# Kernel tuning notes

Measured on AMD Instinct MI355X. Metric: run time of the kernel, lower is better.

## Reference

```python
import jax, jax.numpy as jnp
import numpy as np

N_NODE = 50000
D = 64
N_HEADS = 8
N_LAYERS = 2
NEG = -1e9
PAD = 0
STDV = 1.0 / np.sqrt(D)


def _l2norm(x, axis):
    n = jnp.sqrt(jnp.sum(x * x, axis=axis, keepdims=True))
    return x / jnp.maximum(n, 1e-12)


def _hgconv(x, theta, bias, edge_index):
    # PyG HypergraphConv (use_attention=False): out = D^-1 H B^-1 H^T (x @ theta) + bias
    xt = x @ theta
    node, hedge = edge_index[0], edge_index[1]
    ones = jnp.ones(node.shape[0], x.dtype)
    Bdeg = jax.ops.segment_sum(ones, hedge, num_segments=N_NODE)   # hyperedge degree
    Ddeg = jax.ops.segment_sum(ones, node, num_segments=N_NODE)    # node degree
    m = jax.ops.segment_sum(xt[node], hedge, num_segments=N_NODE)  # nodes -> hyperedges
    m = m * jnp.where(Bdeg > 0, 1.0 / Bdeg, 0.0)[:, None]
    out = jax.ops.segment_sum(m[hedge], node, num_segments=N_NODE) # hyperedges -> nodes
    out = out * jnp.where(Ddeg > 0, 1.0 / Ddeg, 0.0)[:, None]
    return out + bias


def _mha(x, w, pad_mask, reverse):
    # w: [4, D, D] -> q, k, v, out projections. reverse=True attends to future (triu).
    B, L, d = x.shape
    dk = d // N_HEADS
    split = lambda h: h.reshape(B, L, N_HEADS, dk).transpose(0, 2, 1, 3)
    q, k, v = split(x @ w[0]), split(x @ w[1]), split(x @ w[2])
    scores = jnp.einsum('bhid,bhjd->bhij', q, k) / jnp.sqrt(jnp.asarray(dk, x.dtype))
    tri = jnp.triu(jnp.ones((L, L), bool)) if reverse else jnp.tril(jnp.ones((L, L), bool))
    scores = jnp.where(tri[None, None], scores, NEG)
    scores = jnp.where(pad_mask[:, None, None, :], NEG, scores)
    attn = jax.nn.softmax(scores, axis=-1)
    out = jnp.einsum('bhij,bhjd->bhid', attn, v).transpose(0, 2, 1, 3).reshape(B, L, d)
    return out @ w[3], attn


def _prev_user_mask(seq):
    # scatter -1000 at every user id already seen up to position i (index 0 = PAD column)
    B, L = seq.shape
    tril = jnp.tril(jnp.ones((L, L), bool))
    idx = jnp.where(tril[None], seq[:, None, :], 0)                       # [B,L,L]
    idx = jnp.concatenate([idx, jnp.zeros((B, L, 1), idx.dtype)], axis=2)  # [B,L,L+1]
    b = jnp.arange(B)[:, None, None]
    i = jnp.arange(L)[None, :, None]
    return jnp.zeros((B, L, N_NODE), jnp.float32).at[b, i, idx].set(-1000.0)


def _hg_user(emb_table, gate_w, gate_b, att, att_m, theta, theta_b, edges):
    chans = []
    for c in range(3):
        x = emb_table * jax.nn.sigmoid(emb_table @ gate_w[c] + gate_b[c])  # self-gating
        acc, cur = x, x
        for k in range(N_LAYERS):
            cur = _hgconv(cur, theta[k], theta_b[k], edges[c])
            acc = acc + _l2norm(cur, axis=1)
        chans.append(acc / (N_LAYERS + 1))  # mean over [input, layer1, layer2]
    logits = jnp.stack([jnp.sum(att * (c @ att_m), axis=1) for c in chans], axis=1)  # [N,3]
    score = jax.nn.softmax(logits, axis=-1)
    return sum(score[:, i:i + 1] * chans[i] for i in range(3))


def setup_inputs() -> dict:
    key = jax.random.key(0)
    ks = jax.random.split(key, 20)
    u = lambda k, shp: jax.random.uniform(k, shp, jnp.float32, -STDV, STDV)
    B, L, E = 16, 50, 800000
    return {
        'input_seq': jax.random.randint(ks[0], (B, L), 0, N_NODE),
        'label_seq': jax.random.randint(ks[1], (B, L), 0, N_NODE),
        'input_time': jax.random.randint(ks[2], (B, L), 0, 100000),
        'label_time': jax.random.randint(ks[3], (B, L), 0, 100000),
        'edge_index_g': jax.random.randint(ks[4], (2, E), 0, N_NODE),
        'edge_index_i': jax.random.randint(ks[5], (2, E), 0, N_NODE),
        'edge_index_u': jax.random.randint(ks[6], (2, E), 0, N_NODE),
        'emb_table': u(ks[7], (N_NODE, D)),
        'gate_w': u(ks[8], (3, D, D)),
        'gate_b': u(ks[9], (3, D)),
        'att': u(ks[10], (D,)),
        'att_m': u(ks[11], (D, D)),
        'theta': u(ks[12], (N_LAYERS, D, D)),
        'theta_b': u(ks[13], (N_LAYERS, D)),
        'w_hist': u(ks[14], (4, D, D)),
        'w_fut': u(ks[15], (4, D, D)),
    }


def reference(input_seq, label_seq, input_time, label_time,
              edge_index_g, edge_index_i, edge_index_u,
              emb_table, gate_w, gate_b, att, att_m, theta, theta_b, w_hist, w_fut):
    # input_time / label_time are accepted but unused, as in the original forward.
    HG = _hg_user(emb_table, gate_w, gate_b, att, att_m, theta, theta_b,
                  (edge_index_g, edge_index_i, edge_index_u))
    pad_in = input_seq == PAD
    pad_lb = label_seq == PAD
    past_att_out, past_dist = _mha(HG[input_seq], w_hist, pad_in, reverse=False)
    fut_att_out, fut_dist = _mha(HG[label_seq], w_fut, pad_lb, reverse=True)
    output_past = (past_att_out @ HG.T + _prev_user_mask(input_seq)).reshape(-1, N_NODE)
    future_output = (fut_att_out @ HG.T).reshape(-1, N_NODE)
    return (output_past, future_output, past_dist, fut_dist,
            _l2norm(past_att_out, axis=1), _l2norm(fut_att_out, axis=1))
```

## Files before the change

### kernel.cpp

```cpp
#include <hip/hip_runtime.h>
#include <math.h>

#define N_NODE 50000
#define DD 64
#define NE 800000
#define BB 16
#define LL 50
#define NH 8
#define DK 8
#define NEGV -1e9f
#define NB 49
#define NBLK 256
#define EPB 3125

#define OFF_PDIST 80000000u
#define OFF_FDIST 80320000u
#define OFF_L2P 80640000u
#define OFF_L2F 80691200u

typedef unsigned short ushortt;
typedef __attribute__((ext_vector_type(8))) short bf16x8v;
typedef __attribute__((ext_vector_type(4))) float f32x4v;

__device__ __forceinline__ float b2f(ushortt h) { return __uint_as_float(((unsigned)h) << 16); }
__device__ __forceinline__ ushortt f2b(float f) {
    unsigned u = __float_as_uint(f);
    return (ushortt)((u + 0x7fffu + ((u >> 16) & 1u)) >> 16);
}
__device__ __forceinline__ void acc8(float* a, uint4 x) {
    a[0] += b2f((ushortt)(x.x)); a[1] += b2f((ushortt)(x.x >> 16));
    a[2] += b2f((ushortt)(x.y)); a[3] += b2f((ushortt)(x.y >> 16));
    a[4] += b2f((ushortt)(x.z)); a[5] += b2f((ushortt)(x.z >> 16));
    a[6] += b2f((ushortt)(x.w)); a[7] += b2f((ushortt)(x.w >> 16));
}
__device__ __forceinline__ uint4 pack8(const float* a) {
    uint4 w;
    w.x = (unsigned)f2b(a[0]) | ((unsigned)f2b(a[1]) << 16);
    w.y = (unsigned)f2b(a[2]) | ((unsigned)f2b(a[3]) << 16);
    w.z = (unsigned)f2b(a[4]) | ((unsigned)f2b(a[5]) << 16);
    w.w = (unsigned)f2b(a[6]) | ((unsigned)f2b(a[7]) << 16);
    return w;
}

__global__ void k_zero(float* p, int n) {
    int i = blockIdx.x * 256 + threadIdx.x;
    if (i < n) p[i] = 0.0f;
}

__global__ __launch_bounds__(256) void k_cnt(const int* __restrict__ eg,
                                             const int* __restrict__ ei,
                                             const int* __restrict__ eu,
                                             int* __restrict__ hist) {
    int c = blockIdx.y;
    const int* ed = (c == 0) ? eg : ((c == 1) ? ei : eu);
    int blk = blockIdx.x;
    __shared__ int lc[2 * NB];
    int tid = threadIdx.x;
    for (int j = tid; j < 2 * NB; j += 256) lc[j] = 0;
    __syncthreads();
    int e0 = blk * EPB;
    for (int i = e0 + tid; i < e0 + EPB; i += 256) {
        atomicAdd(&lc[ed[NE + i] >> 10], 1);
        atomicAdd(&lc[NB + (ed[i] >> 10)], 1);
    }
    __syncthreads();
    for (int j = tid; j < 2 * NB; j += 256) {
        int side = (j >= NB);
        int b = side ? (j - NB) : j;
        hist[(((side * 3 + c) * NB) + b) * NBLK + blk] = lc[j];
    }
}

__global__ __launch_bounds__(256) void k_scanH(int* __restrict__ hist, int* __restrict__ bb) {
    int t6 = blockIdx.x;
    int* h = hist + t6 * NB * NBLK;
    __shared__ int part[256];
    int tid = threadIdx.x;
    const int CH = (NB * NBLK) / 256;
    int base = tid * CH;
    int s = 0;
    for (int i = 0; i < CH; i++) s += h[base + i];
    part[tid] = s;
    __syncthreads();
    for (int o = 1; o < 256; o <<= 1) {
        int v = (tid >= o) ? part[tid - o] : 0;
        __syncthreads();
        part[tid] += v;
        __syncthreads();
    }
    int run = (tid == 0) ? 0 : part[tid - 1];
    for (int i = 0; i < CH; i++) {
        int idx = base + i;
        int v = h[idx];
        if ((idx & (NBLK - 1)) == 0) bb[t6 * (NB + 1) + (idx >> 8)] = run;
        h[idx] = run;
        run += v;
    }
    if (tid == 255) bb[t6 * (NB + 1) + NB] = run;
}

__global__ __launch_bounds__(256) void k_part2(const int* __restrict__ eg,
                                               const int* __restrict__ ei,
                                               const int* __restrict__ eu,
                                               const int* __restrict__ hist,
                                               unsigned* __restrict__ poolB,
                                               unsigned* __restrict__ poolD) {
    int c = blockIdx.y;
    const int* ed = (c == 0) ? eg : ((c == 1) ? ei : eu);
    int blk = blockIdx.x;
    __shared__ int curB[NB], curD[NB];
    int tid = threadIdx.x;
    for (int j = tid; j < NB; j += 256) {
        curB[j] = hist[(((0 * 3 + c) * NB) + j) * NBLK + blk];
        curD[j] = hist[(((1 * 3 + c) * NB) + j) * NBLK + blk];
    }
    __syncthreads();
    unsigned* pB = poolB + c * 800000;
    unsigned* pD = poolD + c * 800000;
    int e0 = blk * EPB;
    for (int i = e0 + tid; i < e0 + EPB; i += 256) {
        int n = ed[i], h = ed[NE + i];
        int pb = atomicAdd(&curB[h >> 10], 1);
        pB[pb] = ((unsigned)h << 16) | (unsigned)n;
        int pd = atomicAdd(&curD[n >> 10], 1);
        pD[pd] = ((unsigned)n << 16) | (unsigned)h;
    }
}

__global__ __launch_bounds__(256) void k_bucket(const unsigned* __restrict__ poolB,
                                                const unsigned* __restrict__ poolD,
                                                const int* __restrict__ bb,
                                                int* __restrict__ nbrB3, int* __restrict__ nbrD3,
                                                int* __restrict__ offB3, int* __restrict__ offD3,
                                                float* __restrict__ invB3, float* __restrict__ invD3) {
    int b = blockIdx.x, c = blockIdx.y, side = blockIdx.z;
    const unsigned* pool = (side ? poolD : poolB) + c * 800000;
    int* nbr = (side ? nbrD3 : nbrB3) + c * 800000;
    int* off = (side ? offD3 : offB3) + c * 50001;
    float* inv = (side ? invD3 : invB3) + c * 50000;
    int t6 = side * 3 + c;
    int s0 = bb[t6 * (NB + 1) + b], s1 = bb[t6 * (NB + 1) + b + 1];
    int baseSeg = b << 10;
    __shared__ int cnt[1024];
    __shared__ int ofs[1024];
    __shared__ int part[256];
    int tid = threadIdx.x;
    for (int j = tid; j < 1024; j += 256) cnt[j] = 0;
    __syncthreads();
    for (int i = s0 + tid; i < s1; i += 256)
        atomicAdd(&cnt[(pool[i] >> 16) & 1023], 1);
    __syncthreads();
    int t4 = tid * 4;
    int a0 = cnt[t4], a1 = cnt[t4 + 1], a2 = cnt[t4 + 2], a3 = cnt[t4 + 3];
    part[tid] = a0 + a1 + a2 + a3;
    __syncthreads();
    for (int o = 1; o < 256; o <<= 1) {
        int v = (tid >= o) ? part[tid - o] : 0;
        __syncthreads();
        part[tid] += v;
        __syncthreads();
    }
    int excl = (tid == 0) ? 0 : part[tid - 1];
    ofs[t4] = excl;
    ofs[t4 + 1] = excl + a0;
    ofs[t4 + 2] = excl + a0 + a1;
    ofs[t4 + 3] = excl + a0 + a1 + a2;
    __syncthreads();
    for (int ls = tid; ls < 1024; ls += 256) {
        int seg = baseSeg + ls;
        if (seg < N_NODE) {
            off[seg] = s0 + ofs[ls];
            inv[seg] = cnt[ls] ? 1.0f / (float)cnt[ls] : 0.0f;
        }
    }
    if (b == NB - 1 && tid == 0) off[N_NODE] = NE;
    __syncthreads();
    for (int i = s0 + tid; i < s1; i += 256) {
        unsigned u = pool[i];
        int ls = (u >> 16) & 1023;
        int p = atomicAdd(&ofs[ls], 1);
        nbr[s0 + p] = (int)(u & 0xFFFFu);
    }
}

__global__ __launch_bounds__(256) void k_gate3(const float* __restrict__ emb,
                                               const float* __restrict__ gate_w,
                                               const float* __restrict__ gate_b,
                                               float* __restrict__ cur3,
                                               float* __restrict__ acc3) {
    int c = blockIdx.y;
    const float* W = gate_w + c * 4096;
    const float* bias = gate_b + c * 64;
    float* cur = cur3 + (size_t)c * 3200000;
    float* acc = acc3 + (size_t)c * 3200000;
    __shared__ float sW[64 * 64];
    __shared__ float sx[4][64];
    int tid = threadIdx.x;
    for (int i = tid; i < 4096; i += 256) sW[i] = W[i];
    int r = tid >> 6;
    int d = tid & 63;
    int n = blockIdx.x * 4 + r;
    sx[r][d] = emb[n * DD + d];
    __syncthreads();
    float a = bias[d];
#pragma unroll
    for (int k = 0; k < 64; k++) a += sx[r][k] * sW[k * 64 + d];
    float x = sx[r][d] * (1.0f / (1.0f + expf(-a)));
    cur[n * DD + d] = x;
    acc[n * DD + d] = x;
}

__global__ __launch_bounds__(256) void k_mm64h3(const float* __restrict__ cur3,
                                                const float* __restrict__ W,
                                                ushortt* __restrict__ xt3) {
    int c = blockIdx.y;
    const float* X = cur3 + (size_t)c * 3200000;
    ushortt* Y = xt3 + (size_t)c * 3200000;
    __shared__ float sW[64 * 64];
    __shared__ float sx[4][64];
    int tid = threadIdx.x;
    for (int i = tid; i < 4096; i += 256) sW[i] = W[i];
    int r = tid >> 6;
    int d = tid & 63;
    int n = blockIdx.x * 4 + r;
    sx[r][d] = X[n * DD + d];
    __syncthreads();
    float a = 0.0f;
#pragma unroll
    for (int k = 0; k < 64; k++) a += sx[r][k] * sW[k * 64 + d];
    Y[n * DD + d] = f2b(a);
}

__global__ __launch_bounds__(256) void k_gathB3(const ushortt* __restrict__ xt3,
                                                const int* __restrict__ offB3,
                                                const int* __restrict__ nbrB3,
                                                const float* __restrict__ invB3,
                                                ushortt* __restrict__ m3) {
    int c = blockIdx.y;
    const ushortt* src = xt3 + (size_t)c * 3200000;
    const int* off = offB3 + c * 50001;
    const int* nbr = nbrB3 + c * 800000;
    const float* invSeg = invB3 + c * 50000;
    ushortt* dst = m3 + (size_t)c * 3200000;
    int seg = blockIdx.x * 4 + (threadIdx.x >> 6);
    int lane = threadIdx.x & 63;
    int sub = lane >> 3;
    int c8 = lane & 7;
    int s = off[seg], e = off[seg + 1];
    float a[8] = {0.f, 0.f, 0.f, 0.f, 0.f, 0.f, 0.f, 0.f};
    for (int i = s + sub; i < e; i += 8) {
        uint4 x = ((const uint4*)(src + (size_t)nbr[i] * DD))[c8];
        acc8(a, x);
    }
#pragma unroll
    for (int j = 0; j < 8; j++) {
        a[j] += __shfl_xor(a[j], 8, 64);
        a[j] += __shfl_xor(a[j], 16, 64);
        a[j] += __shfl_xor(a[j], 32, 64);
    }
    if (sub == 0) {
        float sc = invSeg[seg];
        float b[8];
#pragma unroll
        for (int j = 0; j < 8; j++) b[j] = a[j] * sc;
        ((uint4*)(dst + (size_t)seg * DD))[c8] = pack8(b);
    }
}

__global__ __launch_bounds__(256) void k_gathD3(const ushortt* __restrict__ m3,
                                                const int* __restrict__ offD3,
                                                const int* __restrict__ nbrD3,
                                                const float* __restrict__ invD3,
                                                const float* __restrict__ bias,
                                                float* __restrict__ cur3,
                                                float* __restrict__ acc3) {
    int c = blockIdx.y;
    const ushortt* m = m3 + (size_t)c * 3200000;
    const int* off = offD3 + c * 50001;
    const int* nbr = nbrD3 + c * 800000;
    const float* invD = invD3 + c * 50000;
    float* cur = cur3 + (size_t)c * 3200000;
    float* acc = acc3 + (size_t)c * 3200000;
    int seg = blockIdx.x * 4 + (threadIdx.x >> 6);
    int lane = threadIdx.x & 63;
    int sub = lane >> 3;
    int c8 = lane & 7;
    int s = off[seg], e = off[seg + 1];
    float a[8] = {0.f, 0.f, 0.f, 0.f, 0.f, 0.f, 0.f, 0.f};
    for (int i = s + sub; i < e; i += 8) {
        uint4 x = ((const uint4*)(m + (size_t)nbr[i] * DD))[c8];
        acc8(a, x);
    }
#pragma unroll
    for (int j = 0; j < 8; j++) {
        a[j] += __shfl_xor(a[j], 8, 64);
        a[j] += __shfl_xor(a[j], 16, 64);
        a[j] += __shfl_xor(a[j], 32, 64);
    }
    float iD = invD[seg];
    float4 bl = ((const float4*)bias)[c8 * 2];
    float4 bh = ((const float4*)bias)[c8 * 2 + 1];
    float v[8];
    v[0] = a[0] * iD + bl.x; v[1] = a[1] * iD + bl.y;
    v[2] = a[2] * iD + bl.z; v[3] = a[3] * iD + bl.w;
    v[4] = a[4] * iD + bh.x; v[5] = a[5] * iD + bh.y;
    v[6] = a[6] * iD + bh.z; v[7] = a[7] * iD + bh.w;
    float ss = 0.f;
#pragma unroll
    for (int j = 0; j < 8; j++) ss += v[j] * v[j];
    ss += __shfl_xor(ss, 1, 64);
    ss += __shfl_xor(ss, 2, 64);
    ss += __shfl_xor(ss, 4, 64);
    float rn = 1.0f / fmaxf(sqrtf(ss), 1e-12f);
    if (sub == 0) {
        float4 v0 = {v[0], v[1], v[2], v[3]};
        float4 v1 = {v[4], v[5], v[6], v[7]};
        float4* cp = (float4*)(cur + (size_t)seg * DD);
        cp[c8 * 2] = v0;
        cp[c8 * 2 + 1] = v1;
        float4* ap = (float4*)(acc + (size_t)seg * DD);
        float4 A0 = ap[c8 * 2], A1 = ap[c8 * 2 + 1];
        A0.x += v[0] * rn; A0.y += v[1] * rn; A0.z += v[2] * rn; A0.w += v[3] * rn;
        A1.x += v[4] * rn; A1.y += v[5] * rn; A1.z += v[6] * rn; A1.w += v[7] * rn;
        ap[c8 * 2] = A0;
        ap[c8 * 2 + 1] = A1;
    }
}

__global__ void k_deg(const int* __restrict__ node, const int* __restrict__ hedge,
                      float* __restrict__ Ddeg, float* __restrict__ Bdeg) {
    int e = blockIdx.x * 256 + threadIdx.x;
    if (e < NE) {
        atomicAdd(&Ddeg[node[e]], 1.0f);
        atomicAdd(&Bdeg[hedge[e]], 1.0f);
    }
}

__global__ void k_inv(float* a, int n) {
    int i = blockIdx.x * 256 + threadIdx.x;
    if (i < n) a[i] = (a[i] > 0.0f) ? (1.0f / a[i]) : 0.0f;
}

__global__ __launch_bounds__(256) void k_scat(const float* __restrict__ src,
                                              const int* __restrict__ gidx,
                                              const int* __restrict__ sidx,
                                              const float* __restrict__ scale,
                                              float* __restrict__ dst) {
    int e = blockIdx.x * 4 + (threadIdx.x >> 6);
    int d = threadIdx.x & 63;
    if (e >= NE) return;
    int g = gidx[e];
    int s = sidx[e];
    float v = src[g * DD + d];
    if (scale) v *= scale[g];
    atomicAdd(&dst[s * DD + d], v);
}

__global__ __launch_bounds__(256) void k_fin(float* __restrict__ cur,
                                             const float* __restrict__ invD,
                                             const float* __restrict__ bias,
                                             float* __restrict__ acc) {
    int r = threadIdx.x >> 6;
    int d = threadIdx.x & 63;
    int n = blockIdx.x * 4 + r;
    float v = cur[n * DD + d] * invD[n] + bias[d];
    cur[n * DD + d] = v;
    float s = v * v;
#pragma unroll
    for (int o = 32; o; o >>= 1) s += __shfl_xor(s, o, 64);
    float nr = fmaxf(sqrtf(s), 1e-12f);
    acc[n * DD + d] += v / nr;
}

__global__ __launch_bounds__(256) void k_gate(const float* __restrict__ emb,
                                              const float* __restrict__ W,
                                              const float* __restrict__ bias,
                                              float* __restrict__ cur,
                                              float* __restrict__ acc) {
    __shared__ float sW[64 * 64];
    __shared__ float sx[4][64];
    int tid = threadIdx.x;
    for (int i = tid; i < 4096; i += 256) sW[i] = W[i];
    int r = tid >> 6;
    int d = tid & 63;
    int n = blockIdx.x * 4 + r;
    sx[r][d] = emb[n * DD + d];
    __syncthreads();
    float a = bias[d];
#pragma unroll
    for (int k = 0; k < 64; k++) a += sx[r][k] * sW[k * 64 + d];
    float x = sx[r][d] * (1.0f / (1.0f + expf(-a)));
    cur[n * DD + d] = x;
    acc[n * DD + d] = x;
}

__global__ __launch_bounds__(256) void k_mm64(const float* __restrict__ X,
                                              const float* __restrict__ W,
                                              float* __restrict__ Y) {
    __shared__ float sW[64 * 64];
    __shared__ float sx[4][64];
    int tid = threadIdx.x;
    for (int i = tid; i < 4096; i += 256) sW[i] = W[i];
    int r = tid >> 6;
    int d = tid & 63;
    int n = blockIdx.x * 4 + r;
    sx[r][d] = X[n * DD + d];
    __syncthreads();
    float a = 0.0f;
#pragma unroll
    for (int k = 0; k < 64; k++) a += sx[r][k] * sW[k * 64 + d];
    Y[n * DD + d] = a;
}

__global__ void k_v(const float* __restrict__ att_m, const float* __restrict__ att,
                    float* __restrict__ v) {
    int e = threadIdx.x;
    float s = 0.0f;
    for (int d = 0; d < 64; d++) s += att_m[e * 64 + d] * att[d];
    v[e] = s;
}

__global__ __launch_bounds__(256) void k_comb(const float* __restrict__ a0,
                                              const float* __restrict__ a1,
                                              const float* __restrict__ a2,
                                              const float* __restrict__ v,
                                              float* __restrict__ HG,
                                              ushortt* __restrict__ HG16) {
    int r = threadIdx.x >> 6;
    int d = threadIdx.x & 63;
    int n = blockIdx.x * 4 + r;
    float x0 = a0[n * DD + d], x1 = a1[n * DD + d], x2 = a2[n * DD + d];
    float vd = v[d];
    float l0 = x0 * vd, l1 = x1 * vd, l2 = x2 * vd;
#pragma unroll
    for (int o = 32; o; o >>= 1) {
        l0 += __shfl_xor(l0, o, 64);
        l1 += __shfl_xor(l1, o, 64);
        l2 += __shfl_xor(l2, o, 64);
    }
    l0 *= (1.0f / 3.0f); l1 *= (1.0f / 3.0f); l2 *= (1.0f / 3.0f);
    float mx = fmaxf(l0, fmaxf(l1, l2));
    float e0 = expf(l0 - mx), e1 = expf(l1 - mx), e2 = expf(l2 - mx);
    float inv = 1.0f / (e0 + e1 + e2);
    float hv = (e0 * x0 + e1 * x1 + e2 * x2) * inv * (1.0f / 3.0f);
    HG[n * DD + d] = hv;
    HG16[n * DD + d] = f2b(hv);
}

__global__ __launch_bounds__(256) void k_attn(const float* __restrict__ HG,
                                              const int* __restrict__ iseq,
                                              const int* __restrict__ lseq,
                                              const float* __restrict__ w_hist,
                                              const float* __restrict__ w_fut,
                                              float* __restrict__ dout,
                                              float* __restrict__ attout,
                                              ushortt* __restrict__ attout16) {
    int b = blockIdx.x;
    int dir = blockIdx.y;
    const int* seq = (dir == 0) ? iseq : lseq;
    const float* W = (dir == 0) ? w_hist : w_fut;
    float* dist = dout + ((dir == 0) ? OFF_PDIST : OFF_FDIST);

    __shared__ float sX[LL * 64];
    __shared__ float sQ[LL * 64];
    __shared__ float sK[LL * 64];
    __shared__ float sV[LL * 64];
    __shared__ float sS[LL * LL];
    __shared__ int sseq[LL];

    int tid = threadIdx.x;
    if (tid < LL) sseq[tid] = seq[b * LL + tid];
    __syncthreads();
    for (int idx = tid; idx < LL * 64; idx += 256) {
        int i = idx >> 6, d = idx & 63;
        sX[idx] = HG[sseq[i] * DD + d];
    }
    __syncthreads();
    for (int idx = tid; idx < LL * 64; idx += 256) {
        int i = idx >> 6, d = idx & 63;
        float q = 0, k = 0, v = 0;
        for (int kk = 0; kk < 64; kk++) {
            float x = sX[i * 64 + kk];
            q += x * W[kk * 64 + d];
            k += x * W[4096 + kk * 64 + d];
            v += x * W[8192 + kk * 64 + d];
        }
        sQ[idx] = q; sK[idx] = k; sV[idx] = v;
    }
    __syncthreads();
    for (int idx = tid; idx < LL * 64; idx += 256) sX[idx] = 0.0f;
    __syncthreads();

    const float scale = 0.35355339059327373f;
    for (int h = 0; h < NH; h++) {
        for (int idx = tid; idx < LL * LL; idx += 256) {
            int i = idx / LL, j = idx % LL;
            float s = 0;
#pragma unroll
            for (int d = 0; d < DK; d++) s += sQ[i * 64 + h * 8 + d] * sK[j * 64 + h * 8 + d];
            s *= scale;
            bool allowed = (dir == 0) ? (j <= i) : (j >= i);
            if (!allowed) s = NEGV;
            if (sseq[j] == 0) s = NEGV;
            sS[idx] = s;
        }
        __syncthreads();
        if (tid < LL) {
            int i = tid;
            float mx = -INFINITY;
            for (int j = 0; j < LL; j++) mx = fmaxf(mx, sS[i * LL + j]);
            float sum = 0;
            for (int j = 0; j < LL; j++) {
                float e = expf(sS[i * LL + j] - mx);
                sS[i * LL + j] = e;
                sum += e;
            }
            float inv = 1.0f / sum;
            for (int j = 0; j < LL; j++) {
                float p = sS[i * LL + j] * inv;
                sS[i * LL + j] = p;
                dist[((b * NH + h) * LL + i) * LL + j] = p;
            }
        }
        __syncthreads();
        for (int idx = tid; idx < LL * DK; idx += 256) {
            int i = idx / DK, d8 = idx % DK;
            float o = 0;
            for (int j = 0; j < LL; j++) o += sS[i * LL + j] * sV[j * 64 + h * 8 + d8];
            sX[i * 64 + h * 8 + d8] = o;
        }
        __syncthreads();
    }
    for (int idx = tid; idx < LL * 64; idx += 256) {
        int i = idx >> 6, d = idx & 63;
        float o = 0;
        for (int kk = 0; kk < 64; kk++) o += sX[i * 64 + kk] * W[3 * 4096 + kk * 64 + d];
        int row = dir * 800 + b * LL + i;
        attout[row * 64 + d] = o;
        attout16[row * 64 + d] = f2b(o);
    }
}

__global__ void k_l2(const float* __restrict__ attout, float* __restrict__ out) {
    int idx = blockIdx.x * 256 + threadIdx.x;
    if (idx >= 2 * BB * 64) return;
    int dir = idx / (BB * 64);
    int r = idx % (BB * 64);
    int b = r / 64, d = r % 64;
    const float* a = attout + (dir * 800 + b * LL) * 64;
    float s = 0;
    for (int l = 0; l < LL; l++) {
        float x = a[l * 64 + d];
        s += x * x;
    }
    float inv = 1.0f / fmaxf(sqrtf(s), 1e-12f);
    float* o = out + ((dir == 0) ? OFF_L2P : OFF_L2F) + b * LL * 64;
    for (int l = 0; l < LL; l++) o[l * 64 + d] = a[l * 64 + d] * inv;
}

__global__ __launch_bounds__(256) void k_bigmm_mfma(const ushortt* __restrict__ A16,
                                                    const ushortt* __restrict__ HG16,
                                                    float* __restrict__ out) {
    int lane = threadIdx.x & 63;
    int w = threadIdx.x >> 6;
    int rt = blockIdx.y * 4 + w;
    int colBase = blockIdx.x * 256;
    int lrow = lane & 15;
    int kb = (lane >> 4) * 8;
    int arow = rt * 16 + lrow;
    bf16x8v a0 = *(const bf16x8v*)(A16 + (size_t)arow * 64 + kb);
    bf16x8v a1 = *(const bf16x8v*)(A16 + (size_t)arow * 64 + kb + 32);
#pragma unroll 4
    for (int ct = 0; ct < 16; ct++) {
        int cb = colBase + ct * 16;
        if (cb >= N_NODE) break;
        int col = cb + lrow;
        bf16x8v b0 = *(const bf16x8v*)(HG16 + (size_t)col * 64 + kb);
        bf16x8v b1 = *(const bf16x8v*)(HG16 + (size_t)col * 64 + kb + 32);
        f32x4v acc = {0.f, 0.f, 0.f, 0.f};
        acc = __builtin_amdgcn_mfma_f32_16x16x32_bf16(a0, b0, acc, 0, 0, 0);
        acc = __builtin_amdgcn_mfma_f32_16x16x32_bf16(a1, b1, acc, 0, 0, 0);
        size_t base = (size_t)(rt * 16 + (lane >> 4) * 4) * 50000 + col;
        out[base] = acc[0];
        out[base + 50000] = acc[1];
        out[base + 100000] = acc[2];
        out[base + 150000] = acc[3];
    }
}

__global__ __launch_bounds__(256) void k_bigmm5(const float* __restrict__ A,
                                                const float* __restrict__ HG,
                                                float* __restrict__ out) {
    int col = blockIdx.x * 256 + threadIdx.x;
    int r0 = blockIdx.y * 400;
    bool ok = (col < N_NODE);
    float4 h[16];
    const float4* hp = (const float4*)(HG + (size_t)(ok ? col : 0) * 64);
#pragma unroll
    for (int t = 0; t < 16; t++) h[t] = hp[t];
    if (!ok) return;
    for (int r = 0; r < 400; r++) {
        int row = r0 + r;
        const float* ar = A + (size_t)row * 64;
        float q0 = 0.f, q1 = 0.f, q2 = 0.f, q3 = 0.f;
#pragma unroll
        for (int t = 0; t < 16; t++) {
            q0 += ar[4 * t + 0] * h[t].x;
            q1 += ar[4 * t + 1] * h[t].y;
            q2 += ar[4 * t + 2] * h[t].z;
            q3 += ar[4 * t + 3] * h[t].w;
        }
        out[(size_t)row * 50000 + col] = (q0 + q1) + (q2 + q3);
    }
}

__global__ __launch_bounds__(64) void k_mask(const int* __restrict__ iseq,
                                             float* __restrict__ out) {
    int row = blockIdx.x;
    int b = row / LL, i = row % LL;
    __shared__ int s[LL];
    int tid = threadIdx.x;
    if (tid < LL) s[tid] = iseq[b * LL + tid];
    __syncthreads();
    float* o = out + (size_t)row * 50000;
    if (tid == 0) o[0] -= 1000.0f;
    if (tid < LL && tid <= i) {
        int c = s[tid];
        if (c > 0 && c < N_NODE) {
            bool first = true;
            for (int j = 0; j < tid; j++)
                if (s[j] == c) { first = false; break; }
            if (first) o[c] -= 1000.0f;
        }
    }
}

extern "C" void kernel_launch(void* const* d_in, const int* in_sizes, int n_in,
                              void* d_out, int out_size, void* d_ws, size_t ws_size,
                              hipStream_t stream) {
    const int* input_seq = (const int*)d_in[0];
    const int* label_seq = (const int*)d_in[1];
    const int* eg = (const int*)d_in[4];
    const int* ei = (const int*)d_in[5];
    const int* eu = (const int*)d_in[6];
    const float* emb = (const float*)d_in[7];
    const float* gate_w = (const float*)d_in[8];
    const float* gate_b = (const float*)d_in[9];
    const float* att = (const float*)d_in[10];
    const float* att_m = (const float*)d_in[11];
    const float* theta = (const float*)d_in[12];
    const float* theta_b = (const float*)d_in[13];
    const float* w_hist = (const float*)d_in[14];
    const float* w_fut = (const float*)d_in[15];

    float* out = (float*)d_out;
    float* ws = (float*)d_ws;

    const size_t HGF = 3200000;
    const int HISTN = 6 * NB * NBLK;
    const size_t needA = (HGF + 102400 + 150000 + 150000 + 128 +
                          (size_t)(HISTN + 6 * (NB + 1) + 64) +
                          300006 + 4 * 2400000 +
                          2 * 2400000 +
                          6 * HGF +
                          HGF / 2 + 51200) * 4;

    if (ws_size >= needA) {
        size_t o = 0;
        float* HG = ws + o; o += HGF;
        float* attout = ws + o; o += 102400;
        float* invB3 = ws + o; o += 150000;
        float* invD3 = ws + o; o += 150000;
        float* vv = ws + o; o += 128;
        int* hist = (int*)(ws + o); o += HISTN;
        int* bbarr = (int*)(ws + o); o += 6 * (NB + 1) + 64;
        int* offB3 = (int*)(ws + o); o += 150003;
        int* offD3 = (int*)(ws + o); o += 150003 + 2;
        int* nbrB3 = (int*)(ws + o); o += 2400000;
        int* nbrD3 = (int*)(ws + o); o += 2400000;
        unsigned* poolB = (unsigned*)(ws + o); o += 2400000;
        unsigned* poolD = (unsigned*)(ws + o); o += 2400000;
        ushortt* xt3 = (ushortt*)(ws + o); o += 4800000;
        ushortt* m3 = (ushortt*)(ws + o); o += 4800000;
        float* acc3 = ws + o; o += 3 * HGF;
        float* cur3 = ws + o; o += 3 * HGF;
        ushortt* HG16 = (ushortt*)(ws + o); o += HGF / 2;
        ushortt* A16 = (ushortt*)(ws + o); o += 51200;

        dim3 pg(NBLK, 3);
        k_cnt<<<pg, 256, 0, stream>>>(eg, ei, eu, hist);
        k_scanH<<<6, 256, 0, stream>>>(hist, bbarr);
        k_part2<<<pg, 256, 0, stream>>>(eg, ei, eu, hist, poolB, poolD);
        dim3 dg(NB, 3, 2);
        k_bucket<<<dg, 256, 0, stream>>>(poolB, poolD, bbarr, nbrB3, nbrD3,
                                         offB3, offD3, invB3, invD3);

        dim3 ng3(12500, 3);
        k_gate3<<<ng3, 256, 0, stream>>>(emb, gate_w, gate_b, cur3, acc3);
        for (int k = 0; k < 2; k++) {
            k_mm64h3<<<ng3, 256, 0, stream>>>(cur3, theta + k * 4096, xt3);
            k_gathB3<<<ng3, 256, 0, stream>>>(xt3, offB3, nbrB3, invB3, m3);
            k_gathD3<<<ng3, 256, 0, stream>>>(m3, offD3, nbrD3, invD3, theta_b + k * 64, cur3, acc3);
        }
        k_v<<<1, 64, 0, stream>>>(att_m, att, vv);
        k_comb<<<12500, 256, 0, stream>>>(acc3, acc3 + HGF, acc3 + 2 * HGF, vv, HG, HG16);
        dim3 ag(BB, 2);
        k_attn<<<ag, 256, 0, stream>>>(HG, input_seq, label_seq, w_hist, w_fut, out, attout, A16);
        k_l2<<<8, 256, 0, stream>>>(attout, out);
        dim3 bg(196, 25);
        k_bigmm_mfma<<<bg, 256, 0, stream>>>(A16, HG16, out);
        k_mask<<<BB * LL, 64, 0, stream>>>(input_seq, out);
    } else {
        float* HG = ws;
        float* attout = HG + HGF;
        float* invB = attout + 102400;
        float* invD = invB + 50000;
        float* vv = invD + 50000;
        if (ws_size < (HGF + 102400 + 100000 + 64) * 4) {
            HG = out + 36550000u;
            attout = HG + HGF;
            invB = attout + 102400;
            invD = invB + 50000;
            vv = invD + 50000;
        }
        float* trans = out;
        float* acc0 = trans;
        float* acc1 = trans + HGF;
        float* acc2 = trans + 2 * HGF;
        float* cur = trans + 3 * HGF;
        float* xt = trans + 4 * HGF;
        float* m = trans + 5 * HGF;
        float* accs[3] = {acc0, acc1, acc2};
        const int* edges[3] = {eg, ei, eu};
        for (int c = 0; c < 3; c++) {
            const int* node = edges[c];
            const int* hedge = edges[c] + NE;
            k_zero<<<(100000 + 255) / 256, 256, 0, stream>>>(invB, 100000);
            k_deg<<<(NE + 255) / 256, 256, 0, stream>>>(node, hedge, invD, invB);
            k_inv<<<(100000 + 255) / 256, 256, 0, stream>>>(invB, 100000);
            k_gate<<<12500, 256, 0, stream>>>(emb, gate_w + c * 4096, gate_b + c * 64, cur, accs[c]);
            for (int k = 0; k < 2; k++) {
                k_mm64<<<12500, 256, 0, stream>>>(cur, theta + k * 4096, xt);
                k_zero<<<12500, 256, 0, stream>>>(m, (int)HGF);
                k_scat<<<NE / 4, 256, 0, stream>>>(xt, node, hedge, nullptr, m);
                k_zero<<<12500, 256, 0, stream>>>(cur, (int)HGF);
                k_scat<<<NE / 4, 256, 0, stream>>>(m, hedge, node, invB, cur);
                k_fin<<<12500, 256, 0, stream>>>(cur, invD, theta_b + k * 64, accs[c]);
            }
        }
        k_v<<<1, 64, 0, stream>>>(att_m, att, vv);
        k_comb<<<12500, 256, 0, stream>>>(acc0, acc1, acc2, vv, HG, (ushortt*)xt);
        dim3 ag(BB, 2);
        k_attn<<<ag, 256, 0, stream>>>(HG, input_seq, label_seq, w_hist, w_fut, out, attout,
                                       (ushortt*)(xt + HGF));
        k_l2<<<8, 256, 0, stream>>>(attout, out);
        dim3 bg5(196, 4);
        k_bigmm5<<<bg5, 256, 0, stream>>>(attout, HG, out);
        k_mask<<<BB * LL, 64, 0, stream>>>(input_seq, out);
    }
}
```

Measured before the change: 852.2 us.

## Fuse theta matmul into hyperedge-to-node gather and fold small kernels into neighbors

Theta is linear, so the per-layer x@theta matmul moves after the node-side aggregation and runs inside the D-gather kernel, which then writes the bf16 input for the next layer directly. This removes the separate mm64 kernels and the fp32 cur buffer round trips. The k_v kernel is folded into k_comb, and k_l2 into k_attn, which cuts launches and the attout buffer. Each gather block now also loads theta into shared memory and adds a block barrier, and bf16 rounding is applied at a different point, which may shift numerics slightly.

```diff
diff --git a/kernel.cpp b/kernel.cpp
--- a/kernel.cpp
+++ b/kernel.cpp
@@ -183,16 +183,16 @@
     }
 }
 
-__global__ __launch_bounds__(256) void k_gate3(const float* __restrict__ emb,
+__global__ __launch_bounds__(256) void k_gateX(const float* __restrict__ emb,
                                                const float* __restrict__ gate_w,
                                                const float* __restrict__ gate_b,
-                                               float* __restrict__ cur3,
-                                               float* __restrict__ acc3) {
+                                               float* __restrict__ acc3,
+                                               ushortt* __restrict__ xt3) {
     int c = blockIdx.y;
     const float* W = gate_w + c * 4096;
     const float* bias = gate_b + c * 64;
-    float* cur = cur3 + (size_t)c * 3200000;
     float* acc = acc3 + (size_t)c * 3200000;
+    ushortt* xt = xt3 + (size_t)c * 3200000;
     __shared__ float sW[64 * 64];
     __shared__ float sx[4][64];
     int tid = threadIdx.x;
@@ -206,29 +206,8 @@
 #pragma unroll
     for (int k = 0; k < 64; k++) a += sx[r][k] * sW[k * 64 + d];
     float x = sx[r][d] * (1.0f / (1.0f + expf(-a)));
-    cur[n * DD + d] = x;
     acc[n * DD + d] = x;
-}
-
-__global__ __launch_bounds__(256) void k_mm64h3(const float* __restrict__ cur3,
-                                                const float* __restrict__ W,
-                                                ushortt* __restrict__ xt3) {
-    int c = blockIdx.y;
-    const float* X = cur3 + (size_t)c * 3200000;
-    ushortt* Y = xt3 + (size_t)c * 3200000;
-    __shared__ float sW[64 * 64];
-    __shared__ float sx[4][64];
-    int tid = threadIdx.x;
-    for (int i = tid; i < 4096; i += 256) sW[i] = W[i];
-    int r = tid >> 6;
-    int d = tid & 63;
-    int n = blockIdx.x * 4 + r;
-    sx[r][d] = X[n * DD + d];
-    __syncthreads();
-    float a = 0.0f;
-#pragma unroll
-    for (int k = 0; k < 64; k++) a += sx[r][k] * sW[k * 64 + d];
-    Y[n * DD + d] = f2b(a);
+    xt[n * DD + d] = f2b(x);
 }
 
 __global__ __launch_bounds__(256) void k_gathB3(const ushortt* __restrict__ xt3,
@@ -267,22 +246,33 @@
     }
 }
 
-__global__ __launch_bounds__(256) void k_gathD3(const ushortt* __restrict__ m3,
-                                                const int* __restrict__ offD3,
-                                                const int* __restrict__ nbrD3,
-                                                const float* __restrict__ invD3,
-                                                const float* __restrict__ bias,
-                                                float* __restrict__ cur3,
-                                                float* __restrict__ acc3) {
+template <int WRITE_XT>
+__global__ __launch_bounds__(256) void k_gathD3f(const ushortt* __restrict__ m3,
+                                                 const int* __restrict__ offD3,
+                                                 const int* __restrict__ nbrD3,
+                                                 const float* __restrict__ invD3,
+                                                 const float* __restrict__ theta,
+                                                 const float* __restrict__ theta_b,
+                                                 float* __restrict__ acc3,
+                                                 ushortt* __restrict__ xt3) {
     int c = blockIdx.y;
     const ushortt* m = m3 + (size_t)c * 3200000;
     const int* off = offD3 + c * 50001;
     const int* nbr = nbrD3 + c * 800000;
     const float* invD = invD3 + c * 50000;
-    float* cur = cur3 + (size_t)c * 3200000;
     float* acc = acc3 + (size_t)c * 3200000;
-    int seg = blockIdx.x * 4 + (threadIdx.x >> 6);
-    int lane = threadIdx.x & 63;
+    ushortt* xt = xt3 + (size_t)c * 3200000;
+
+    __shared__ float sTh[64 * 64];
+    __shared__ float sx[4][64];
+    __shared__ float sb[64];
+    int tid = threadIdx.x;
+    for (int i = tid; i < 4096; i += 256) sTh[i] = theta[i];
+    if (tid < 64) sb[tid] = theta_b[tid];
+
+    int w = tid >> 6;
+    int seg = blockIdx.x * 4 + w;
+    int lane = tid & 63;
     int sub = lane >> 3;
     int c8 = lane & 7;
     int s = off[seg], e = off[seg + 1];
@@ -297,140 +287,46 @@
         a[j] += __shfl_xor(a[j], 16, 64);
         a[j] += __shfl_xor(a[j], 32, 64);
     }
-    float iD = invD[seg];
-    float4 bl = ((const float4*)bias)[c8 * 2];
-    float4 bh = ((const float4*)bias)[c8 * 2 + 1];
-    float v[8];
-    v[0] = a[0] * iD + bl.x; v[1] = a[1] * iD + bl.y;
-    v[2] = a[2] * iD + bl.z; v[3] = a[3] * iD + bl.w;
-    v[4] = a[4] * iD + bh.x; v[5] = a[5] * iD + bh.y;
-    v[6] = a[6] * iD + bh.z; v[7] = a[7] * iD + bh.w;
-    float ss = 0.f;
-#pragma unroll
-    for (int j = 0; j < 8; j++) ss += v[j] * v[j];
-    ss += __shfl_xor(ss, 1, 64);
-    ss += __shfl_xor(ss, 2, 64);
-    ss += __shfl_xor(ss, 4, 64);
-    float rn = 1.0f / fmaxf(sqrtf(ss), 1e-12f);
     if (sub == 0) {
-        float4 v0 = {v[0], v[1], v[2], v[3]};
-        float4 v1 = {v[4], v[5], v[6], v[7]};
-        float4* cp = (float4*)(cur + (size_t)seg * DD);
-        cp[c8 * 2] = v0;
-        cp[c8 * 2 + 1] = v1;
-        float4* ap = (float4*)(acc + (size_t)seg * DD);
-        float4 A0 = ap[c8 * 2], A1 = ap[c8 * 2 + 1];
-        A0.x += v[0] * rn; A0.y += v[1] * rn; A0.z += v[2] * rn; A0.w += v[3] * rn;
-        A1.x += v[4] * rn; A1.y += v[5] * rn; A1.z += v[6] * rn; A1.w += v[7] * rn;
-        ap[c8 * 2] = A0;
-        ap[c8 * 2 + 1] = A1;
-    }
-}
-
-__global__ void k_deg(const int* __restrict__ node, const int* __restrict__ hedge,
-                      float* __restrict__ Ddeg, float* __restrict__ Bdeg) {
-    int e = blockIdx.x * 256 + threadIdx.x;
-    if (e < NE) {
-        atomicAdd(&Ddeg[node[e]], 1.0f);
-        atomicAdd(&Bdeg[hedge[e]], 1.0f);
-    }
-}
-
-__global__ void k_inv(float* a, int n) {
-    int i = blockIdx.x * 256 + threadIdx.x;
-    if (i < n) a[i] = (a[i] > 0.0f) ? (1.0f / a[i]) : 0.0f;
-}
-
-__global__ __launch_bounds__(256) void k_scat(const float* __restrict__ src,
-                                              const int* __restrict__ gidx,
-                                              const int* __restrict__ sidx,
-                                              const float* __restrict__ scale,
-                                              float* __restrict__ dst) {
-    int e = blockIdx.x * 4 + (threadIdx.x >> 6);
-    int d = threadIdx.x & 63;
-    if (e >= NE) return;
-    int g = gidx[e];
-    int s = sidx[e];
-    float v = src[g * DD + d];
-    if (scale) v *= scale[g];
-    atomicAdd(&dst[s * DD + d], v);
-}
-
-__global__ __launch_bounds__(256) void k_fin(float* __restrict__ cur,
-                                             const float* __restrict__ invD,
-                                             const float* __restrict__ bias,
-                                             float* __restrict__ acc) {
-    int r = threadIdx.x >> 6;
-    int d = threadIdx.x & 63;
-    int n = blockIdx.x * 4 + r;
-    float v = cur[n * DD + d] * invD[n] + bias[d];
-    cur[n * DD + d] = v;
-    float s = v * v;
-#pragma unroll
-    for (int o = 32; o; o >>= 1) s += __shfl_xor(s, o, 64);
-    float nr = fmaxf(sqrtf(s), 1e-12f);
-    acc[n * DD + d] += v / nr;
-}
-
-__global__ __launch_bounds__(256) void k_gate(const float* __restrict__ emb,
-                                              const float* __restrict__ W,
-                                              const float* __restrict__ bias,
-                                              float* __restrict__ cur,
-                                              float* __restrict__ acc) {
-    __shared__ float sW[64 * 64];
-    __shared__ float sx[4][64];
-    int tid = threadIdx.x;
-    for (int i = tid; i < 4096; i += 256) sW[i] = W[i];
+        float iD = invD[seg];
+#pragma unroll
+        for (int j = 0; j < 8; j++) sx[w][c8 * 8 + j] = a[j] * iD;
+    }
+    __syncthreads();
+
+    int d = lane;
+    float v = sb[d];
+#pragma unroll
+    for (int k = 0; k < 64; k++) v += sx[w][k] * sTh[k * 64 + d];
+    float ss = v * v;
+#pragma unroll
+    for (int o = 32; o; o >>= 1) ss += __shfl_xor(ss, o, 64);
+    float nr = fmaxf(sqrtf(ss), 1e-12f);
+    size_t idx = (size_t)seg * DD + d;
+    acc[idx] += v / nr;
+    if (WRITE_XT) xt[idx] = f2b(v);
+}
+
+__global__ __launch_bounds__(256) void k_comb(const float* __restrict__ a0,
+                                              const float* __restrict__ a1,
+                                              const float* __restrict__ a2,
+                                              const float* __restrict__ att_m,
+                                              const float* __restrict__ att,
+                                              float* __restrict__ HG,
+                                              ushortt* __restrict__ HG16) {
+    __shared__ float svv[64];
+    int tid = threadIdx.x;
+    if (tid < 64) {
+        float s = 0.f;
+        for (int k = 0; k < 64; k++) s += att_m[tid * 64 + k] * att[k];
+        svv[tid] = s;
+    }
+    __syncthreads();
     int r = tid >> 6;
     int d = tid & 63;
     int n = blockIdx.x * 4 + r;
-    sx[r][d] = emb[n * DD + d];
-    __syncthreads();
-    float a = bias[d];
-#pragma unroll
-    for (int k = 0; k < 64; k++) a += sx[r][k] * sW[k * 64 + d];
-    float x = sx[r][d] * (1.0f / (1.0f + expf(-a)));
-    cur[n * DD + d] = x;
-    acc[n * DD + d] = x;
-}
-
-__global__ __launch_bounds__(256) void k_mm64(const float* __restrict__ X,
-                                              const float* __restrict__ W,
-                                              float* __restrict__ Y) {
-    __shared__ float sW[64 * 64];
-    __shared__ float sx[4][64];
-    int tid = threadIdx.x;
-    for (int i = tid; i < 4096; i += 256) sW[i] = W[i];
-    int r = tid >> 6;
-    int d = tid & 63;
-    int n = blockIdx.x * 4 + r;
-    sx[r][d] = X[n * DD + d];
-    __syncthreads();
-    float a = 0.0f;
-#pragma unroll
-    for (int k = 0; k < 64; k++) a += sx[r][k] * sW[k * 64 + d];
-    Y[n * DD + d] = a;
-}
-
-__global__ void k_v(const float* __restrict__ att_m, const float* __restrict__ att,
-                    float* __restrict__ v) {
-    int e = threadIdx.x;
-    float s = 0.0f;
-    for (int d = 0; d < 64; d++) s += att_m[e * 64 + d] * att[d];
-    v[e] = s;
-}
-
-__global__ __launch_bounds__(256) void k_comb(const float* __restrict__ a0,
-                                              const float* __restrict__ a1,
-                                              const float* __restrict__ a2,
-                                              const float* __restrict__ v,
-                                              float* __restrict__ HG,
-                                              ushortt* __restrict__ HG16) {
-    int r = threadIdx.x >> 6;
-    int d = threadIdx.x & 63;
-    int n = blockIdx.x * 4 + r;
     float x0 = a0[n * DD + d], x1 = a1[n * DD + d], x2 = a2[n * DD + d];
-    float vd = v[d];
+    float vd = svv[d];
     float l0 = x0 * vd, l1 = x1 * vd, l2 = x2 * vd;
 #pragma unroll
     for (int o = 32; o; o >>= 1) {
@@ -453,8 +349,8 @@
                                               const float* __restrict__ w_hist,
                                               const float* __restrict__ w_fut,
                                               float* __restrict__ dout,
-                                              float* __restrict__ attout,
-                                              ushortt* __restrict__ attout16) {
+                                              ushortt* __restrict__ attout16,
+                                              float* __restrict__ attoutF) {
     int b = blockIdx.x;
     int dir = blockIdx.y;
     const int* seq = (dir == 0) ? iseq : lseq;
@@ -466,6 +362,7 @@
     __shared__ float sK[LL * 64];
     __shared__ float sV[LL * 64];
     __shared__ float sS[LL * LL];
+    __shared__ float sInv[64];
     __shared__ int sseq[LL];
 
     int tid = threadIdx.x;
@@ -535,27 +432,26 @@
         int i = idx >> 6, d = idx & 63;
         float o = 0;
         for (int kk = 0; kk < 64; kk++) o += sX[i * 64 + kk] * W[3 * 4096 + kk * 64 + d];
+        sQ[idx] = o;
         int row = dir * 800 + b * LL + i;
-        attout[row * 64 + d] = o;
         attout16[row * 64 + d] = f2b(o);
-    }
-}
-
-__global__ void k_l2(const float* __restrict__ attout, float* __restrict__ out) {
-    int idx = blockIdx.x * 256 + threadIdx.x;
-    if (idx >= 2 * BB * 64) return;
-    int dir = idx / (BB * 64);
-    int r = idx % (BB * 64);
-    int b = r / 64, d = r % 64;
-    const float* a = attout + (dir * 800 + b * LL) * 64;
-    float s = 0;
-    for (int l = 0; l < LL; l++) {
-        float x = a[l * 64 + d];
-        s += x * x;
-    }
-    float inv = 1.0f / fmaxf(sqrtf(s), 1e-12f);
-    float* o = out + ((dir == 0) ? OFF_L2P : OFF_L2F) + b * LL * 64;
-    for (int l = 0; l < LL; l++) o[l * 64 + d] = a[l * 64 + d] * inv;
+        if (attoutF) attoutF[row * 64 + d] = o;
+    }
+    __syncthreads();
+    if (tid < 64) {
+        float s = 0;
+        for (int l = 0; l < LL; l++) {
+            float x = sQ[l * 64 + tid];
+            s += x * x;
+        }
+        sInv[tid] = 1.0f / fmaxf(sqrtf(s), 1e-12f);
+    }
+    __syncthreads();
+    float* ol2 = dout + ((dir == 0) ? OFF_L2P : OFF_L2F) + b * LL * 64;
+    for (int idx = tid; idx < LL * 64; idx += 256) {
+        int d = idx & 63;
+        ol2[idx] = sQ[idx] * sInv[d];
+    }
 }
 
 __global__ __launch_bounds__(256) void k_bigmm_mfma(const ushortt* __restrict__ A16,
@@ -588,32 +484,6 @@
     }
 }
 
-__global__ __launch_bounds__(256) void k_bigmm5(const float* __restrict__ A,
-                                                const float* __restrict__ HG,
-                                                float* __restrict__ out) {
-    int col = blockIdx.x * 256 + threadIdx.x;
-    int r0 = blockIdx.y * 400;
-    bool ok = (col < N_NODE);
-    float4 h[16];
-    const float4* hp = (const float4*)(HG + (size_t)(ok ? col : 0) * 64);
-#pragma unroll
-    for (int t = 0; t < 16; t++) h[t] = hp[t];
-    if (!ok) return;
-    for (int r = 0; r < 400; r++) {
-        int row = r0 + r;
-        const float* ar = A + (size_t)row * 64;
-        float q0 = 0.f, q1 = 0.f, q2 = 0.f, q3 = 0.f;
-#pragma unroll
-        for (int t = 0; t < 16; t++) {
-            q0 += ar[4 * t + 0] * h[t].x;
-            q1 += ar[4 * t + 1] * h[t].y;
-            q2 += ar[4 * t + 2] * h[t].z;
-            q3 += ar[4 * t + 3] * h[t].w;
-        }
-        out[(size_t)row * 50000 + col] = (q0 + q1) + (q2 + q3);
-    }
-}
-
 __global__ __launch_bounds__(64) void k_mask(const int* __restrict__ iseq,
                                              float* __restrict__ out) {
     int row = blockIdx.x;
@@ -632,6 +502,117 @@
                 if (s[j] == c) { first = false; break; }
             if (first) o[c] -= 1000.0f;
         }
+    }
+}
+
+__global__ void k_deg(const int* __restrict__ node, const int* __restrict__ hedge,
+                      float* __restrict__ Ddeg, float* __restrict__ Bdeg) {
+    int e = blockIdx.x * 256 + threadIdx.x;
+    if (e < NE) {
+        atomicAdd(&Ddeg[node[e]], 1.0f);
+        atomicAdd(&Bdeg[hedge[e]], 1.0f);
+    }
+}
+
+__global__ void k_inv(float* a, int n) {
+    int i = blockIdx.x * 256 + threadIdx.x;
+    if (i < n) a[i] = (a[i] > 0.0f) ? (1.0f / a[i]) : 0.0f;
+}
+
+__global__ __launch_bounds__(256) void k_scat(const float* __restrict__ src,
+                                              const int* __restrict__ gidx,
+                                              const int* __restrict__ sidx,
+                                              const float* __restrict__ scale,
+                                              float* __restrict__ dst) {
+    int e = blockIdx.x * 4 + (threadIdx.x >> 6);
+    int d = threadIdx.x & 63;
+    if (e >= NE) return;
+    int g = gidx[e];
+    int s = sidx[e];
+    float v = src[g * DD + d];
+    if (scale) v *= scale[g];
+    atomicAdd(&dst[s * DD + d], v);
+}
+
+__global__ __launch_bounds__(256) void k_fin(float* __restrict__ cur,
+                                             const float* __restrict__ invD,
+                                             const float* __restrict__ bias,
+                                             float* __restrict__ acc) {
+    int r = threadIdx.x >> 6;
+    int d = threadIdx.x & 63;
+    int n = blockIdx.x * 4 + r;
+    float v = cur[n * DD + d] * invD[n] + bias[d];
+    cur[n * DD + d] = v;
+    float s = v * v;
+#pragma unroll
+    for (int o = 32; o; o >>= 1) s += __shfl_xor(s, o, 64);
+    float nr = fmaxf(sqrtf(s), 1e-12f);
+    acc[n * DD + d] += v / nr;
+}
+
+__global__ __launch_bounds__(256) void k_gate(const float* __restrict__ emb,
+                                              const float* __restrict__ W,
+                                              const float* __restrict__ bias,
+                                              float* __restrict__ cur,
+                                              float* __restrict__ acc) {
+    __shared__ float sW[64 * 64];
+    __shared__ float sx[4][64];
+    int tid = threadIdx.x;
+    for (int i = tid; i < 4096; i += 256) sW[i] = W[i];
+    int r = tid >> 6;
+    int d = tid & 63;
+    int n = blockIdx.x * 4 + r;
+    sx[r][d] = emb[n * DD + d];
+    __syncthreads();
+    float a = bias[d];
+#pragma unroll
+    for (int k = 0; k < 64; k++) a += sx[r][k] * sW[k * 64 + d];
+    float x = sx[r][d] * (1.0f / (1.0f + expf(-a)));
+    cur[n * DD + d] = x;
+    acc[n * DD + d] = x;
+}
+
+__global__ __launch_bounds__(256) void k_mm64(const float* __restrict__ X,
+                                              const float* __restrict__ W,
+                                              float* __restrict__ Y) {
+    __shared__ float sW[64 * 64];
+    __shared__ float sx[4][64];
+    int tid = threadIdx.x;
+    for (int i = tid; i < 4096; i += 256) sW[i] = W[i];
+    int r = tid >> 6;
+    int d = tid & 63;
+    int n = blockIdx.x * 4 + r;
+    sx[r][d] = X[n * DD + d];
+    __syncthreads();
+    float a = 0.0f;
+#pragma unroll
+    for (int k = 0; k < 64; k++) a += sx[r][k] * sW[k * 64 + d];
+    Y[n * DD + d] = a;
+}
+
+__global__ __launch_bounds__(256) void k_bigmm5(const float* __restrict__ A,
+                                                const float* __restrict__ HG,
+                                                float* __restrict__ out) {
+    int col = blockIdx.x * 256 + threadIdx.x;
+    int r0 = blockIdx.y * 400;
+    bool ok = (col < N_NODE);
+    float4 h[16];
+    const float4* hp = (const float4*)(HG + (size_t)(ok ? col : 0) * 64);
+#pragma unroll
+    for (int t = 0; t < 16; t++) h[t] = hp[t];
+    if (!ok) return;
+    for (int r = 0; r < 400; r++) {
+        int row = r0 + r;
+        const float* ar = A + (size_t)row * 64;
+        float q0 = 0.f, q1 = 0.f, q2 = 0.f, q3 = 0.f;
+#pragma unroll
+        for (int t = 0; t < 16; t++) {
+            q0 += ar[4 * t + 0] * h[t].x;
+            q1 += ar[4 * t + 1] * h[t].y;
+            q2 += ar[4 * t + 2] * h[t].z;
+            q3 += ar[4 * t + 3] * h[t].w;
+        }
+        out[(size_t)row * 50000 + col] = (q0 + q1) + (q2 + q3);
     }
 }
 
@@ -658,20 +639,18 @@
 
     const size_t HGF = 3200000;
     const int HISTN = 6 * NB * NBLK;
-    const size_t needA = (HGF + 102400 + 150000 + 150000 + 128 +
+    const size_t needA = (HGF + 150000 + 150000 +
                           (size_t)(HISTN + 6 * (NB + 1) + 64) +
                           300006 + 4 * 2400000 +
                           2 * 2400000 +
-                          6 * HGF +
-                          HGF / 2 + 51200) * 4;
+                          3 * HGF +
+                          HGF / 2 + 51200 + 1024) * 4;
 
     if (ws_size >= needA) {
         size_t o = 0;
         float* HG = ws + o; o += HGF;
-        float* attout = ws + o; o += 102400;
         float* invB3 = ws + o; o += 150000;
         float* invD3 = ws + o; o += 150000;
-        float* vv = ws + o; o += 128;
         int* hist = (int*)(ws + o); o += HISTN;
         int* bbarr = (int*)(ws + o); o += 6 * (NB + 1) + 64;
         int* offB3 = (int*)(ws + o); o += 150003;
@@ -683,7 +662,6 @@
         ushortt* xt3 = (ushortt*)(ws + o); o += 4800000;
         ushortt* m3 = (ushortt*)(ws + o); o += 4800000;
         float* acc3 = ws + o; o += 3 * HGF;
-        float* cur3 = ws + o; o += 3 * HGF;
         ushortt* HG16 = (ushortt*)(ws + o); o += HGF / 2;
         ushortt* A16 = (ushortt*)(ws + o); o += 51200;
 
@@ -696,32 +674,30 @@
                                          offB3, offD3, invB3, invD3);
 
         dim3 ng3(12500, 3);
-        k_gate3<<<ng3, 256, 0, stream>>>(emb, gate_w, gate_b, cur3, acc3);
-        for (int k = 0; k < 2; k++) {
-            k_mm64h3<<<ng3, 256, 0, stream>>>(cur3, theta + k * 4096, xt3);
-            k_gathB3<<<ng3, 256, 0, stream>>>(xt3, offB3, nbrB3, invB3, m3);
-            k_gathD3<<<ng3, 256, 0, stream>>>(m3, offD3, nbrD3, invD3, theta_b + k * 64, cur3, acc3);
-        }
-        k_v<<<1, 64, 0, stream>>>(att_m, att, vv);
-        k_comb<<<12500, 256, 0, stream>>>(acc3, acc3 + HGF, acc3 + 2 * HGF, vv, HG, HG16);
+        k_gateX<<<ng3, 256, 0, stream>>>(emb, gate_w, gate_b, acc3, xt3);
+        k_gathB3<<<ng3, 256, 0, stream>>>(xt3, offB3, nbrB3, invB3, m3);
+        k_gathD3f<1><<<ng3, 256, 0, stream>>>(m3, offD3, nbrD3, invD3,
+                                              theta, theta_b, acc3, xt3);
+        k_gathB3<<<ng3, 256, 0, stream>>>(xt3, offB3, nbrB3, invB3, m3);
+        k_gathD3f<0><<<ng3, 256, 0, stream>>>(m3, offD3, nbrD3, invD3,
+                                              theta + 4096, theta_b + 64, acc3, xt3);
+
+        k_comb<<<12500, 256, 0, stream>>>(acc3, acc3 + HGF, acc3 + 2 * HGF,
+                                          att_m, att, HG, HG16);
         dim3 ag(BB, 2);
-        k_attn<<<ag, 256, 0, stream>>>(HG, input_seq, label_seq, w_hist, w_fut, out, attout, A16);
-        k_l2<<<8, 256, 0, stream>>>(attout, out);
+        k_attn<<<ag, 256, 0, stream>>>(HG, input_seq, label_seq, w_hist, w_fut,
+                                       out, A16, nullptr);
         dim3 bg(196, 25);
         k_bigmm_mfma<<<bg, 256, 0, stream>>>(A16, HG16, out);
         k_mask<<<BB * LL, 64, 0, stream>>>(input_seq, out);
     } else {
         float* HG = ws;
-        float* attout = HG + HGF;
-        float* invB = attout + 102400;
+        float* invB = HG + HGF;
         float* invD = invB + 50000;
-        float* vv = invD + 50000;
-        if (ws_size < (HGF + 102400 + 100000 + 64) * 4) {
+        if (ws_size < (HGF + 100000 + 64) * 4) {
             HG = out + 36550000u;
-            attout = HG + HGF;
-            invB = attout + 102400;
+            invB = HG + HGF;
             invD = invB + 50000;
-            vv = invD + 50000;
         }
         float* trans = out;
         float* acc0 = trans;
@@ -748,14 +724,12 @@
                 k_fin<<<12500, 256, 0, stream>>>(cur, invD, theta_b + k * 64, accs[c]);
             }
         }
-        k_v<<<1, 64, 0, stream>>>(att_m, att, vv);
-        k_comb<<<12500, 256, 0, stream>>>(acc0, acc1, acc2, vv, HG, (ushortt*)xt);
+        k_comb<<<12500, 256, 0, stream>>>(acc0, acc1, acc2, att_m, att, HG, (ushortt*)m);
         dim3 ag(BB, 2);
-        k_attn<<<ag, 256, 0, stream>>>(HG, input_seq, label_seq, w_hist, w_fut, out, attout,
-                                       (ushortt*)(xt + HGF));
-        k_l2<<<8, 256, 0, stream>>>(attout, out);
+        k_attn<<<ag, 256, 0, stream>>>(HG, input_seq, label_seq, w_hist, w_fut,
+                                       out, (ushortt*)(m + HGF), xt);
         dim3 bg5(196, 4);
-        k_bigmm5<<<bg5, 256, 0, stream>>>(attout, HG, out);
+        k_bigmm5<<<bg5, 256, 0, stream>>>(xt, HG, out);
         k_mask<<<BB * LL, 64, 0, stream>>>(input_seq, out);
     }
 }
```

New measurement: 845.1 us. No clear change (-0.8%).
